# Performance work log

Hardware: AMD Instinct MI355X
Metric: run time of the kernel (lower is better)

The kernel has to match this reference:

```python
import jax, jax.numpy as jnp
import numpy as np

B, S, D = 4, 2048, 1024
LN_EPS = 1e-3  # keras LayerNormalization default


def setup_inputs() -> dict:
    key = jax.random.key(0)
    ks = jax.random.split(key, 4)
    std = 1.0 / np.sqrt(D)
    return {
        "inputs": jax.random.normal(ks[0], (B, S, D), dtype=jnp.float32),
        "Wq": jax.random.normal(ks[1], (D, D), dtype=jnp.float32) * std,
        "bq": jnp.zeros((D,), jnp.float32),
        "Wk": jax.random.normal(ks[2], (D, D), dtype=jnp.float32) * std,
        "bk": jnp.zeros((D,), jnp.float32),
        "Wv": jax.random.normal(ks[3], (D, D), dtype=jnp.float32) * std,
        "bv": jnp.zeros((D,), jnp.float32),
        "ln_gamma": jnp.ones((D,), jnp.float32),
        "ln_beta": jnp.zeros((D,), jnp.float32),
    }


def reference(inputs, Wq, bq, Wk, bk, Wv, bv, ln_gamma, ln_beta):
    d = inputs.shape[-1]
    scale = jnp.sqrt(jnp.asarray(d, inputs.dtype))
    q = inputs @ Wq + bq          # [B,S,D]
    k = inputs @ Wk + bk
    v = inputs @ Wv + bv
    scores = jnp.einsum("bqd,bkd->bqk", q, k) / scale  # [B,S,S]
    attn = jax.nn.softmax(scores, axis=-1)
    context = jnp.einsum("bqk,bkd->bqd", attn, v)      # [B,S,D]
    resid = context + inputs
    mu = jnp.mean(resid, axis=-1, keepdims=True)
    var = jnp.mean(jnp.square(resid - mu), axis=-1, keepdims=True)
    normed = (resid - mu) * jax.lax.rsqrt(var + LN_EPS)
    return normed * ln_gamma + ln_beta
```

## Files before the change

### kernel.cpp

```cpp
#include <hip/hip_runtime.h>
#include <hip/hip_bf16.h>
#include <cstdint>
#include <cstddef>


typedef unsigned short u16;
using bf16x8 = __attribute__((ext_vector_type(8))) short;
using f32x16 = __attribute__((ext_vector_type(16))) float;

typedef __attribute__((address_space(3))) unsigned int lds_uint;
typedef const __attribute__((address_space(1))) unsigned int glob_uint;

__device__ __forceinline__ float bf2f(u16 h) {
    union { unsigned int u; float f; } c;
    c.u = ((unsigned int)h) << 16;
    return c.f;
}
__device__ __forceinline__ u16 f2bf(float f) {
    union { float f; unsigned int u; } c;
    c.f = f;
    return (u16)((c.u + 0x7fffu + ((c.u >> 16) & 1u)) >> 16);
}
__device__ __forceinline__ void load_lds16(const void* g, void* l) {
    __builtin_amdgcn_global_load_lds((glob_uint*)g, (lds_uint*)l, 16, 0, 0);
}

__device__ __forceinline__ int detect_fp32(const u16* X, int* sflag) {
    const int t = threadIdx.x;
    if (t < 64) {
        bool bad = false, nz = false;
#pragma unroll
        for (int j = 0; j < 4; ++j) {
            float v = bf2f(X[(t * 4 + j) * 2]);
            if (!(fabsf(v) <= 1e9f)) bad = true;
            if (v != 0.f) nz = true;
        }
        unsigned long long ab = __ballot(bad);
        unsigned long long an = __ballot(nz);
        if (t == 0) *sflag = (ab != 0ull || an == 0ull) ? 1 : 0;
    }
    __syncthreads();
    return *sflag;
}

__global__ __launch_bounds__(256) void prep_kernel(
    const void* __restrict__ X, const void* __restrict__ Wq,
    const void* __restrict__ Wk, const void* __restrict__ Wv,
    const void* __restrict__ bq, const void* __restrict__ bk,
    const void* __restrict__ bv, const void* __restrict__ gamma,
    const void* __restrict__ beta,
    u16* __restrict__ Xb, u16* __restrict__ Wt, u16* __restrict__ bias5)
{
    __shared__ u16 tile[64][72];
    __shared__ int sflag;
    const int fp32 = detect_fp32((const u16*)X, &sflag);
    const int t   = threadIdx.x;
    const int blk = blockIdx.x;

    if (blk < 4096) {
        const size_t i = ((size_t)blk * 256 + t) * 8;
        if (fp32) {
            const float* f = (const float*)X;
            float4 a = *(const float4*)(f + i);
            float4 b = *(const float4*)(f + i + 4);
            ushort4 o0, o1;
            o0.x = f2bf(a.x); o0.y = f2bf(a.y); o0.z = f2bf(a.z); o0.w = f2bf(a.w);
            o1.x = f2bf(b.x); o1.y = f2bf(b.y); o1.z = f2bf(b.z); o1.w = f2bf(b.w);
            *(ushort4*)(Xb + i) = o0;
            *(ushort4*)(Xb + i + 4) = o1;
        } else {
            *(uint4*)(Xb + i) = *(const uint4*)((const u16*)X + i);
        }
    } else if (blk < 4864) {
        const int idx = blk - 4096;
        const int k0 = (idx & 15) * 64;
        const int n0 = ((idx >> 4) & 15) * 64;
        const int w  = idx >> 8;
        const void* W = (w == 0) ? Wq : ((w == 1) ? Wk : Wv);
#pragma unroll
        for (int it = 0; it < 2; ++it) {
            int i2 = t + it * 256;
            int r = i2 >> 3;
            int c = (i2 & 7) * 8;
            const size_t off = (size_t)(k0 + r) * 1024 + n0 + c;
            if (fp32) {
                const float* Wf = (const float*)W + off;
                float4 a = *(const float4*)Wf;
                float4 b = *(const float4*)(Wf + 4);
                u16* tp = &tile[r][c];
                tp[0] = f2bf(a.x); tp[1] = f2bf(a.y); tp[2] = f2bf(a.z); tp[3] = f2bf(a.w);
                tp[4] = f2bf(b.x); tp[5] = f2bf(b.y); tp[6] = f2bf(b.z); tp[7] = f2bf(b.w);
            } else {
                *(uint4*)&tile[r][c] = *(const uint4*)((const u16*)W + off);
            }
        }
        __syncthreads();
#pragma unroll
        for (int it = 0; it < 2; ++it) {
            int i2 = t + it * 256;
            int r = i2 >> 3;
            int c = (i2 & 7) * 8;
            union { u16 s[8]; uint4 v; } tmp;
#pragma unroll
            for (int j = 0; j < 8; ++j) tmp.s[j] = tile[c + j][r];
            *(uint4*)(Wt + (size_t)(w * 1024 + n0 + r) * 1024 + k0 + c) = tmp.v;
        }
    } else {
        const int v = blk - 4864;
        const void* srcs[5] = {bq, bk, bv, gamma, beta};
        const void* src = srcs[v];
        u16* d = bias5 + (size_t)v * 1024;
        const int i = t * 4;
        if (fp32) {
            const float* f = (const float*)src;
            ushort4 o;
            o.x = f2bf(f[i]); o.y = f2bf(f[i + 1]);
            o.z = f2bf(f[i + 2]); o.w = f2bf(f[i + 3]);
            *(ushort4*)(d + i) = o;
        } else {
            *(ushort4*)(d + i) = *(const ushort4*)((const u16*)src + i);
        }
    }
}

__global__ __launch_bounds__(256) void transpose_v4_kernel(
    const u16* __restrict__ QKV, u16* __restrict__ Vt4)
{
    __shared__ u16 tile[64][72];
    const int t  = threadIdx.x;
    const int k0 = blockIdx.x * 64;
    const int n0 = blockIdx.y * 64;
    const int b  = blockIdx.z;
    const u16* Vsrc = QKV + (size_t)b * 2048 * 3072 + 2048;
    u16* Vt = Vt4 + (size_t)b * 1024 * 2048;
#pragma unroll
    for (int it = 0; it < 2; ++it) {
        int idx = t + it * 256;
        int r = idx >> 3;
        int c = (idx & 7) * 8;
        *(uint4*)&tile[r][c] = *(const uint4*)(Vsrc + (size_t)(k0 + r) * 3072 + n0 + c);
    }
    __syncthreads();
#pragma unroll
    for (int it = 0; it < 2; ++it) {
        int idx = t + it * 256;
        int r = idx >> 3;
        int c = (idx & 7) * 8;
        union { u16 s[8]; uint4 v; } tmp;
#pragma unroll
        for (int j = 0; j < 8; ++j) tmp.s[j] = tile[c + j][r];
        *(uint4*)(Vt + (size_t)(n0 + r) * 2048 + k0 + c) = tmp.v;
    }
}

template<int EPI, int BN>
__global__ __launch_bounds__(512, 2) void gemm256(
    const u16* __restrict__ A, int lda, size_t sA,
    const u16* __restrict__ Bt, int ldb, size_t sB,
    u16* __restrict__ C, int ldc, size_t sC,
    int K, float scale, const u16* __restrict__ bias3)
{
    constexpr int WAVES_M = (BN == 256) ? 2 : 4;
    constexpr int WM = 256 / WAVES_M;
    constexpr int MF = WM / 32;
    __shared__ u16 As[4][256 * 32];
    __shared__ u16 Bs[4][BN * 32];

    const int t  = threadIdx.x;
    const int l  = t & 63;
    const int w  = t >> 6;
    const int wm = (BN == 256) ? (w >> 2) : (w >> 1);
    const int wn = (BN == 256) ? (w & 3)  : (w & 1);
    const int m0 = blockIdx.y * 256;
    const int n0 = blockIdx.x * BN;
    A  += (size_t)blockIdx.z * sA;
    Bt += (size_t)blockIdx.z * sB;
    C  += (size_t)blockIdx.z * sC;

    const int sa = (t & 3) ^ ((t >> 3) & 3);
    const u16* Ag0 = A  + (size_t)(m0 + (t >> 2)) * lda + sa * 8;
    const u16* Ag1 = Ag0 + (size_t)128 * lda;
    const u16* Bg0 = Bt + (size_t)(n0 + (t >> 2)) * ldb + sa * 8;
    const u16* Bg1 = Bg0 + (size_t)128 * ldb;

    const int lr   = l & 31;
    const int key  = (lr >> 1) & 3;
    const int sp0  = (l >> 5) ^ key;
    const int aoff = (wm * WM + lr) * 32;
    const int boff = (wn * 64 + lr) * 32;

    f32x16 acc[MF][2];
#pragma unroll
    for (int mi = 0; mi < MF; ++mi)
#pragma unroll
        for (int ni = 0; ni < 2; ++ni)
#pragma unroll
            for (int r = 0; r < 16; ++r) acc[mi][ni][r] = 0.f;

    const int NS = K >> 5;

    auto stage = [&](int j, int sl) {
        const size_t ko = (size_t)j * 32;
        load_lds16(Ag0 + ko, &As[sl][w * 512]);
        load_lds16(Ag1 + ko, &As[sl][4096 + w * 512]);
        load_lds16(Bg0 + ko, &Bs[sl][w * 512]);
        if constexpr (BN == 256) load_lds16(Bg1 + ko, &Bs[sl][4096 + w * 512]);
    };

    stage(0, 0); stage(1, 1); stage(2, 2);
    if constexpr (BN == 256) asm volatile("s_waitcnt vmcnt(8)" ::: "memory");
    else                     asm volatile("s_waitcnt vmcnt(6)" ::: "memory");
    __builtin_amdgcn_s_barrier();
    asm volatile("" ::: "memory");

    for (int j = 0; j < NS; ++j) {
        const int sl = j & 3;
        bf16x8 a[MF][2], b[2][2];
        const u16* as_ = &As[sl][aoff];
        const u16* bs_ = &Bs[sl][boff];
#pragma unroll
        for (int ks = 0; ks < 2; ++ks) {
            const int sp = (ks ? (sp0 ^ 2) : sp0) * 8;
#pragma unroll
            for (int mi = 0; mi < MF; ++mi)
                a[mi][ks] = *(const bf16x8*)(as_ + mi * 1024 + sp);
#pragma unroll
            for (int ni = 0; ni < 2; ++ni)
                b[ni][ks] = *(const bf16x8*)(bs_ + ni * 1024 + sp);
        }
        if (j + 3 < NS) stage(j + 3, (j + 3) & 3);
        const int rem = NS - 2 - j;
        if (rem >= 2) {
            if constexpr (BN == 256) asm volatile("s_waitcnt vmcnt(8)" ::: "memory");
            else                     asm volatile("s_waitcnt vmcnt(6)" ::: "memory");
        } else if (rem == 1) {
            if constexpr (BN == 256) asm volatile("s_waitcnt vmcnt(4)" ::: "memory");
            else                     asm volatile("s_waitcnt vmcnt(3)" ::: "memory");
        } else if (rem == 0) {
            asm volatile("s_waitcnt vmcnt(0)" ::: "memory");
        }
        if (j + 1 < NS) {
            __builtin_amdgcn_s_barrier();
            asm volatile("" ::: "memory");
        }
        __builtin_amdgcn_s_setprio(1);
#pragma unroll
        for (int ks = 0; ks < 2; ++ks)
#pragma unroll
            for (int mi = 0; mi < MF; ++mi)
#pragma unroll
                for (int ni = 0; ni < 2; ++ni)
                    acc[mi][ni] = __builtin_amdgcn_mfma_f32_32x32x16_bf16(
                        a[mi][ks], b[ni][ks], acc[mi][ni], 0, 0, 0);
        __builtin_amdgcn_s_setprio(0);
        if (j + 1 < NS) {
            __builtin_amdgcn_s_barrier();
            asm volatile("" ::: "memory");
        }
    }

    const int colb = n0 + wn * 64 + lr;
    const int rowb = m0 + wm * WM + 4 * (l >> 5);
#pragma unroll
    for (int mi = 0; mi < MF; ++mi) {
#pragma unroll
        for (int ni = 0; ni < 2; ++ni) {
            const int col = colb + ni * 32;
            const float bias = (EPI == 0) ? bf2f(bias3[col]) : 0.f;
#pragma unroll
            for (int r = 0; r < 16; ++r) {
                const int row = rowb + mi * 32 + (r & 3) + 8 * (r >> 2);
                C[(size_t)row * ldc + col] = f2bf(acc[mi][ni][r] * scale + bias);
            }
        }
    }
}

__global__ __launch_bounds__(256) void softmax_bf16_kernel(u16* __restrict__ S)
{
    const int t = threadIdx.x;
    u16* sp = S + (size_t)blockIdx.x * 2048;
    union { uint4 v; u16 h[8]; } raw;
    raw.v = *(const uint4*)(sp + t * 8);
    float vals[8];
#pragma unroll
    for (int i = 0; i < 8; ++i) vals[i] = bf2f(raw.h[i]);
    float m = vals[0];
#pragma unroll
    for (int i = 1; i < 8; ++i) m = fmaxf(m, vals[i]);
#pragma unroll
    for (int off = 32; off > 0; off >>= 1) m = fmaxf(m, __shfl_xor(m, off));
    __shared__ float red[8];
    const int w = t >> 6, lane = t & 63;
    if (lane == 0) red[w] = m;
    __syncthreads();
    m = fmaxf(fmaxf(red[0], red[1]), fmaxf(red[2], red[3]));
    float e[8], s = 0.f;
#pragma unroll
    for (int i = 0; i < 8; ++i) { e[i] = __expf(vals[i] - m); s += e[i]; }
#pragma unroll
    for (int off = 32; off > 0; off >>= 1) s += __shfl_xor(s, off);
    if (lane == 0) red[4 + w] = s;
    __syncthreads();
    s = red[4] + red[5] + red[6] + red[7];
    const float rinv = 1.f / s;
    union { uint4 v; u16 h[8]; } out;
#pragma unroll
    for (int i = 0; i < 8; ++i) out.h[i] = f2bf(e[i] * rinv);
    *(uint4*)(sp + t * 8) = out.v;
}

__global__ __launch_bounds__(256) void resid_ln_kernel(
    const u16* __restrict__ Ctx, const u16* __restrict__ Xb,
    const u16* __restrict__ gamma, const u16* __restrict__ beta,
    void* __restrict__ Out, const u16* __restrict__ Xraw)
{
    __shared__ int sflag;
    const int fp32 = detect_fp32(Xraw, &sflag);
    const size_t row = blockIdx.x;
    const int t = threadIdx.x;
    ushort4 cv = *(const ushort4*)(Ctx + row * 3072 + t * 4);
    ushort4 xv = *(const ushort4*)(Xb + row * 1024 + t * 4);
    float v[4] = {bf2f(cv.x) + bf2f(xv.x), bf2f(cv.y) + bf2f(xv.y),
                  bf2f(cv.z) + bf2f(xv.z), bf2f(cv.w) + bf2f(xv.w)};
    float s  = v[0] + v[1] + v[2] + v[3];
    float s2 = v[0] * v[0] + v[1] * v[1] + v[2] * v[2] + v[3] * v[3];
#pragma unroll
    for (int off = 32; off > 0; off >>= 1) {
        s  += __shfl_xor(s, off);
        s2 += __shfl_xor(s2, off);
    }
    __shared__ float red[8];
    const int w = t >> 6, lane = t & 63;
    if (lane == 0) { red[w] = s; red[4 + w] = s2; }
    __syncthreads();
    s  = red[0] + red[1] + red[2] + red[3];
    s2 = red[4] + red[5] + red[6] + red[7];
    const float mu  = s * (1.f / 1024.f);
    const float var = s2 * (1.f / 1024.f) - mu * mu;
    const float inv = rsqrtf(var + 1e-3f);
    ushort4 gv = *(const ushort4*)(gamma + t * 4);
    ushort4 bv = *(const ushort4*)(beta + t * 4);
    float o[4];
    o[0] = (v[0] - mu) * inv * bf2f(gv.x) + bf2f(bv.x);
    o[1] = (v[1] - mu) * inv * bf2f(gv.y) + bf2f(bv.y);
    o[2] = (v[2] - mu) * inv * bf2f(gv.z) + bf2f(bv.z);
    o[3] = (v[3] - mu) * inv * bf2f(gv.w) + bf2f(bv.w);
    if (fp32) {
        float4 fo = {o[0], o[1], o[2], o[3]};
        *(float4*)((float*)Out + row * 1024 + t * 4) = fo;
    } else {
        ushort4 bo;
        bo.x = f2bf(o[0]); bo.y = f2bf(o[1]); bo.z = f2bf(o[2]); bo.w = f2bf(o[3]);
        *(ushort4*)((u16*)Out + row * 1024 + t * 4) = bo;
    }
}

extern "C" void kernel_launch(void* const* d_in, const int* in_sizes, int n_in,
                              void* d_out, int out_size, void* d_ws, size_t ws_size,
                              hipStream_t stream)
{
    (void)in_sizes; (void)n_in; (void)out_size; (void)ws_size;
    const void* X     = d_in[0];
    const void* Wq    = d_in[1];
    const void* bq    = d_in[2];
    const void* Wk    = d_in[3];
    const void* bk    = d_in[4];
    const void* Wv    = d_in[5];
    const void* bv    = d_in[6];
    const void* gamma = d_in[7];
    const void* beta  = d_in[8];

    char* ws = (char*)d_ws;
    u16* bias5 = (u16*)(ws + 16);
    u16* Wt    = (u16*)(ws + 16384);
    u16* QKV   = (u16*)(ws + 6307840);
    u16* Xb    = (u16*)(ws + 56639488);
    u16* S4    = (u16*)(ws + 73416704);
    u16* Vt4   = (u16*)(ws + 106971136);

    prep_kernel<<<4869, 256, 0, stream>>>(
        X, Wq, Wk, Wv, bq, bk, bv, gamma, beta, Xb, Wt, bias5);

    gemm256<0, 128><<<dim3(24, 32, 1), 512, 0, stream>>>(
        Xb, 1024, 0, Wt, 1024, 0, QKV, 3072, 0, 1024, 1.f, bias5);

    gemm256<1, 256><<<dim3(8, 8, 4), 512, 0, stream>>>(
        QKV, 3072, (size_t)2048 * 3072,
        QKV + 1024, 3072, (size_t)2048 * 3072,
        S4, 2048, (size_t)2048 * 2048, 1024, 0.03125f, nullptr);

    softmax_bf16_kernel<<<8192, 256, 0, stream>>>(S4);

    transpose_v4_kernel<<<dim3(32, 16, 4), 256, 0, stream>>>(QKV, Vt4);

    gemm256<1, 128><<<dim3(8, 8, 4), 512, 0, stream>>>(
        S4, 2048, (size_t)2048 * 2048,
        Vt4, 2048, (size_t)1024 * 2048,
        QKV, 3072, (size_t)2048 * 3072, 2048, 1.f, nullptr);

    resid_ln_kernel<<<8192, 256, 0, stream>>>(
        QKV, Xb, bias5 + 3 * 1024, bias5 + 4 * 1024, d_out, (const u16*)X);
}
```

Before: 298.5 us.

## Rework GEMM to 256x256 tiles with BK=64 double buffering and split-K PV

Replaces the templated GEMM with a single 256x256-tile kernel that stages K in 64-wide slabs into two LDS buffers, using a new XOR swizzle, instead of a 4-deep pipeline of 32-wide slabs. The attention-times-V GEMM is split along K into two halves. Each half writes its partial context into a separate 1024-column slot of the QKV buffer, and the residual+LayerNorm kernel sums the two partials. The aim is more MFMA work per barrier and better grid fill for the PV product. The cost is a shallower prefetch pipeline, an extra partial-sum read, and summing the partials in bf16.

```diff
diff --git a/kernel.cpp b/kernel.cpp
--- a/kernel.cpp
+++ b/kernel.cpp
@@ -153,116 +153,122 @@
     }
 }
 
-template<int EPI, int BN>
-__global__ __launch_bounds__(512, 2) void gemm256(
+template<int EPI, int KSPLIT>
+__global__ __launch_bounds__(512, 2) void gemm256r(
     const u16* __restrict__ A, int lda, size_t sA,
     const u16* __restrict__ Bt, int ldb, size_t sB,
     u16* __restrict__ C, int ldc, size_t sC,
     int K, float scale, const u16* __restrict__ bias3)
 {
-    constexpr int WAVES_M = (BN == 256) ? 2 : 4;
-    constexpr int WM = 256 / WAVES_M;
-    constexpr int MF = WM / 32;
-    __shared__ u16 As[4][256 * 32];
-    __shared__ u16 Bs[4][BN * 32];
+    __shared__ u16 As[2][256 * 64];
+    __shared__ u16 Bs[2][256 * 64];
 
     const int t  = threadIdx.x;
     const int l  = t & 63;
     const int w  = t >> 6;
-    const int wm = (BN == 256) ? (w >> 2) : (w >> 1);
-    const int wn = (BN == 256) ? (w & 3)  : (w & 1);
+    const int wm = w >> 2;
+    const int wn = w & 3;
     const int m0 = blockIdx.y * 256;
-    const int n0 = blockIdx.x * BN;
-    A  += (size_t)blockIdx.z * sA;
-    Bt += (size_t)blockIdx.z * sB;
-    C  += (size_t)blockIdx.z * sC;
-
-    const int sa = (t & 3) ^ ((t >> 3) & 3);
-    const u16* Ag0 = A  + (size_t)(m0 + (t >> 2)) * lda + sa * 8;
-    const u16* Ag1 = Ag0 + (size_t)128 * lda;
-    const u16* Bg0 = Bt + (size_t)(n0 + (t >> 2)) * ldb + sa * 8;
-    const u16* Bg1 = Bg0 + (size_t)128 * ldb;
+    const int n0 = blockIdx.x * 256;
+    const int batch = (int)blockIdx.z >> (KSPLIT - 1);
+    const int ks    = (int)blockIdx.z & (KSPLIT - 1);
+    A  += (size_t)batch * sA + (size_t)ks * K;
+    Bt += (size_t)batch * sB + (size_t)ks * K;
+    C  += (size_t)batch * sC + (size_t)ks * 1024;
+
+    const int srow = w * 8 + (l >> 3);
+    const int sg   = (l & 7) ^ (l >> 3);
+    const u16* Ag = A  + (size_t)(m0 + srow) * lda + sg * 8;
+    const u16* Bg = Bt + (size_t)(n0 + srow) * ldb + sg * 8;
+
+    auto stage = [&](int j, int buf) {
+        const size_t kb = (size_t)j * 64;
+        const u16* ag = Ag + kb;
+        const u16* bg = Bg + kb;
+        u16* al = &As[buf][w * 512];
+        u16* bl = &Bs[buf][w * 512];
+#pragma unroll
+        for (int i = 0; i < 4; ++i) {
+            load_lds16(ag + (size_t)i * 64 * lda, al + i * 4096);
+            load_lds16(bg + (size_t)i * 64 * ldb, bl + i * 4096);
+        }
+    };
 
     const int lr   = l & 31;
-    const int key  = (lr >> 1) & 3;
-    const int sp0  = (l >> 5) ^ key;
-    const int aoff = (wm * WM + lr) * 32;
-    const int boff = (wn * 64 + lr) * 32;
-
-    f32x16 acc[MF][2];
-#pragma unroll
-    for (int mi = 0; mi < MF; ++mi)
+    const int kh   = l >> 5;
+    const int keyr = lr & 7;
+    const int aoff = (wm * 128 + lr) * 64;
+    const int boff = (wn * 64 + lr) * 64;
+
+    f32x16 acc[4][2];
+#pragma unroll
+    for (int mi = 0; mi < 4; ++mi)
 #pragma unroll
         for (int ni = 0; ni < 2; ++ni)
 #pragma unroll
             for (int r = 0; r < 16; ++r) acc[mi][ni][r] = 0.f;
 
-    const int NS = K >> 5;
-
-    auto stage = [&](int j, int sl) {
-        const size_t ko = (size_t)j * 32;
-        load_lds16(Ag0 + ko, &As[sl][w * 512]);
-        load_lds16(Ag1 + ko, &As[sl][4096 + w * 512]);
-        load_lds16(Bg0 + ko, &Bs[sl][w * 512]);
-        if constexpr (BN == 256) load_lds16(Bg1 + ko, &Bs[sl][4096 + w * 512]);
-    };
-
-    stage(0, 0); stage(1, 1); stage(2, 2);
-    if constexpr (BN == 256) asm volatile("s_waitcnt vmcnt(8)" ::: "memory");
-    else                     asm volatile("s_waitcnt vmcnt(6)" ::: "memory");
+    const int NS = K >> 6;
+
+    stage(0, 0);
+    stage(1, 1);
+    asm volatile("s_waitcnt vmcnt(8)" ::: "memory");
     __builtin_amdgcn_s_barrier();
     asm volatile("" ::: "memory");
 
     for (int j = 0; j < NS; ++j) {
-        const int sl = j & 3;
-        bf16x8 a[MF][2], b[2][2];
-        const u16* as_ = &As[sl][aoff];
-        const u16* bs_ = &Bs[sl][boff];
-#pragma unroll
-        for (int ks = 0; ks < 2; ++ks) {
-            const int sp = (ks ? (sp0 ^ 2) : sp0) * 8;
-#pragma unroll
-            for (int mi = 0; mi < MF; ++mi)
-                a[mi][ks] = *(const bf16x8*)(as_ + mi * 1024 + sp);
-#pragma unroll
-            for (int ni = 0; ni < 2; ++ni)
-                b[ni][ks] = *(const bf16x8*)(bs_ + ni * 1024 + sp);
-        }
-        if (j + 3 < NS) stage(j + 3, (j + 3) & 3);
-        const int rem = NS - 2 - j;
-        if (rem >= 2) {
-            if constexpr (BN == 256) asm volatile("s_waitcnt vmcnt(8)" ::: "memory");
-            else                     asm volatile("s_waitcnt vmcnt(6)" ::: "memory");
-        } else if (rem == 1) {
-            if constexpr (BN == 256) asm volatile("s_waitcnt vmcnt(4)" ::: "memory");
-            else                     asm volatile("s_waitcnt vmcnt(3)" ::: "memory");
-        } else if (rem == 0) {
+        const int buf = j & 1;
+        const u16* as_ = &As[buf][aoff];
+        const u16* bs_ = &Bs[buf][boff];
+        bf16x8 a[4][4], b[2][4];
+#pragma unroll
+        for (int ks2 = 0; ks2 < 2; ++ks2) {
+            const int sp = ((ks2 * 2 + kh) ^ keyr) * 8;
+#pragma unroll
+            for (int mi = 0; mi < 4; ++mi) a[mi][ks2] = *(const bf16x8*)(as_ + mi * 2048 + sp);
+#pragma unroll
+            for (int ni = 0; ni < 2; ++ni) b[ni][ks2] = *(const bf16x8*)(bs_ + ni * 2048 + sp);
+        }
+        if (j + 1 < NS) stage(j + 1, buf ^ 1);
+        __builtin_amdgcn_s_setprio(1);
+#pragma unroll
+        for (int ks2 = 0; ks2 < 2; ++ks2)
+#pragma unroll
+            for (int mi = 0; mi < 4; ++mi)
+#pragma unroll
+                for (int ni = 0; ni < 2; ++ni)
+                    acc[mi][ni] = __builtin_amdgcn_mfma_f32_32x32x16_bf16(
+                        a[mi][ks2], b[ni][ks2], acc[mi][ni], 0, 0, 0);
+        __builtin_amdgcn_s_setprio(0);
+#pragma unroll
+        for (int ks2 = 2; ks2 < 4; ++ks2) {
+            const int sp = ((ks2 * 2 + kh) ^ keyr) * 8;
+#pragma unroll
+            for (int mi = 0; mi < 4; ++mi) a[mi][ks2] = *(const bf16x8*)(as_ + mi * 2048 + sp);
+#pragma unroll
+            for (int ni = 0; ni < 2; ++ni) b[ni][ks2] = *(const bf16x8*)(bs_ + ni * 2048 + sp);
+        }
+        __builtin_amdgcn_s_setprio(1);
+#pragma unroll
+        for (int ks2 = 2; ks2 < 4; ++ks2)
+#pragma unroll
+            for (int mi = 0; mi < 4; ++mi)
+#pragma unroll
+                for (int ni = 0; ni < 2; ++ni)
+                    acc[mi][ni] = __builtin_amdgcn_mfma_f32_32x32x16_bf16(
+                        a[mi][ks2], b[ni][ks2], acc[mi][ni], 0, 0, 0);
+        __builtin_amdgcn_s_setprio(0);
+        if (j + 1 < NS) {
             asm volatile("s_waitcnt vmcnt(0)" ::: "memory");
-        }
-        if (j + 1 < NS) {
             __builtin_amdgcn_s_barrier();
             asm volatile("" ::: "memory");
         }
-        __builtin_amdgcn_s_setprio(1);
-#pragma unroll
-        for (int ks = 0; ks < 2; ++ks)
-#pragma unroll
-            for (int mi = 0; mi < MF; ++mi)
-#pragma unroll
-                for (int ni = 0; ni < 2; ++ni)
-                    acc[mi][ni] = __builtin_amdgcn_mfma_f32_32x32x16_bf16(
-                        a[mi][ks], b[ni][ks], acc[mi][ni], 0, 0, 0);
-        __builtin_amdgcn_s_setprio(0);
-        if (j + 1 < NS) {
-            __builtin_amdgcn_s_barrier();
-            asm volatile("" ::: "memory");
-        }
     }
 
     const int colb = n0 + wn * 64 + lr;
-    const int rowb = m0 + wm * WM + 4 * (l >> 5);
-#pragma unroll
-    for (int mi = 0; mi < MF; ++mi) {
+    const int rowb = m0 + wm * 128 + 4 * kh;
+#pragma unroll
+    for (int mi = 0; mi < 4; ++mi) {
 #pragma unroll
         for (int ni = 0; ni < 2; ++ni) {
             const int col = colb + ni * 32;
@@ -319,10 +325,13 @@
     const int fp32 = detect_fp32(Xraw, &sflag);
     const size_t row = blockIdx.x;
     const int t = threadIdx.x;
-    ushort4 cv = *(const ushort4*)(Ctx + row * 3072 + t * 4);
-    ushort4 xv = *(const ushort4*)(Xb + row * 1024 + t * 4);
-    float v[4] = {bf2f(cv.x) + bf2f(xv.x), bf2f(cv.y) + bf2f(xv.y),
-                  bf2f(cv.z) + bf2f(xv.z), bf2f(cv.w) + bf2f(xv.w)};
+    ushort4 cv0 = *(const ushort4*)(Ctx + row * 3072 + t * 4);
+    ushort4 cv1 = *(const ushort4*)(Ctx + row * 3072 + 1024 + t * 4);
+    ushort4 xv  = *(const ushort4*)(Xb + row * 1024 + t * 4);
+    float v[4] = {bf2f(cv0.x) + bf2f(cv1.x) + bf2f(xv.x),
+                  bf2f(cv0.y) + bf2f(cv1.y) + bf2f(xv.y),
+                  bf2f(cv0.z) + bf2f(cv1.z) + bf2f(xv.z),
+                  bf2f(cv0.w) + bf2f(cv1.w) + bf2f(xv.w)};
     float s  = v[0] + v[1] + v[2] + v[3];
     float s2 = v[0] * v[0] + v[1] * v[1] + v[2] * v[2] + v[3] * v[3];
 #pragma unroll
@@ -382,10 +391,10 @@
     prep_kernel<<<4869, 256, 0, stream>>>(
         X, Wq, Wk, Wv, bq, bk, bv, gamma, beta, Xb, Wt, bias5);
 
-    gemm256<0, 128><<<dim3(24, 32, 1), 512, 0, stream>>>(
+    gemm256r<0, 1><<<dim3(12, 32, 1), 512, 0, stream>>>(
         Xb, 1024, 0, Wt, 1024, 0, QKV, 3072, 0, 1024, 1.f, bias5);
 
-    gemm256<1, 256><<<dim3(8, 8, 4), 512, 0, stream>>>(
+    gemm256r<1, 1><<<dim3(8, 8, 4), 512, 0, stream>>>(
         QKV, 3072, (size_t)2048 * 3072,
         QKV + 1024, 3072, (size_t)2048 * 3072,
         S4, 2048, (size_t)2048 * 2048, 1024, 0.03125f, nullptr);
@@ -394,10 +403,10 @@
 
     transpose_v4_kernel<<<dim3(32, 16, 4), 256, 0, stream>>>(QKV, Vt4);
 
-    gemm256<1, 128><<<dim3(8, 8, 4), 512, 0, stream>>>(
+    gemm256r<1, 2><<<dim3(4, 8, 8), 512, 0, stream>>>(
         S4, 2048, (size_t)2048 * 2048,
         Vt4, 2048, (size_t)1024 * 2048,
-        QKV, 3072, (size_t)2048 * 3072, 2048, 1.f, nullptr);
+        QKV, 3072, (size_t)2048 * 3072, 1024, 1.f, nullptr);
 
     resid_ln_kernel<<<8192, 256, 0, stream>>>(
         QKV, Xb, bias5 + 3 * 1024, bias5 + 4 * 1024, d_out, (const u16*)X);
```

Measured after the change: 287.6 us. 3.7% less time.

## Rewrite GEMM with K=64 stages, triple buffering and interleaved LDS loads/MFMA

Applied to the files above, without the earlier changes.

Replaces the templated GEMM with a single 256x128 tile kernel that stages K in chunks of 64 rather than 32. It uses a 3-slot LDS ring instead of 4 and an 8-way XOR swizzle. LDS fragment reads are interleaved with the MFMA groups to hide LDS latency, and there are half as many barriers per K element. The QK^T GEMM now uses 256x128 tiles with twice the grid instead of 256x256. The cost is larger per-stage LDS (~144KB total), which may limit occupancy to one block per CU despite launch_bounds(512,2).

```diff
diff --git a/kernel.cpp b/kernel.cpp
--- a/kernel.cpp
+++ b/kernel.cpp
@@ -153,116 +153,133 @@
     }
 }
 
-template<int EPI, int BN>
-__global__ __launch_bounds__(512, 2) void gemm256(
+#define MFMA4(A0, A1, B0, B1)                                                   \
+    __builtin_amdgcn_s_setprio(1);                                              \
+    acc[0][0] = __builtin_amdgcn_mfma_f32_32x32x16_bf16(A0, B0, acc[0][0], 0, 0, 0); \
+    acc[0][1] = __builtin_amdgcn_mfma_f32_32x32x16_bf16(A0, B1, acc[0][1], 0, 0, 0); \
+    acc[1][0] = __builtin_amdgcn_mfma_f32_32x32x16_bf16(A1, B0, acc[1][0], 0, 0, 0); \
+    acc[1][1] = __builtin_amdgcn_mfma_f32_32x32x16_bf16(A1, B1, acc[1][1], 0, 0, 0); \
+    __builtin_amdgcn_s_setprio(0);
+
+template<int EPI>
+__global__ __launch_bounds__(512, 2) void gemm256x128(
     const u16* __restrict__ A, int lda, size_t sA,
     const u16* __restrict__ Bt, int ldb, size_t sB,
     u16* __restrict__ C, int ldc, size_t sC,
     int K, float scale, const u16* __restrict__ bias3)
 {
-    constexpr int WAVES_M = (BN == 256) ? 2 : 4;
-    constexpr int WM = 256 / WAVES_M;
-    constexpr int MF = WM / 32;
-    __shared__ u16 As[4][256 * 32];
-    __shared__ u16 Bs[4][BN * 32];
+    __shared__ u16 As[3][256 * 64];
+    __shared__ u16 Bs[3][128 * 64];
 
     const int t  = threadIdx.x;
     const int l  = t & 63;
     const int w  = t >> 6;
-    const int wm = (BN == 256) ? (w >> 2) : (w >> 1);
-    const int wn = (BN == 256) ? (w & 3)  : (w & 1);
+    const int wm = w >> 1;
+    const int wn = w & 1;
     const int m0 = blockIdx.y * 256;
-    const int n0 = blockIdx.x * BN;
+    const int n0 = blockIdx.x * 128;
     A  += (size_t)blockIdx.z * sA;
     Bt += (size_t)blockIdx.z * sB;
     C  += (size_t)blockIdx.z * sC;
 
-    const int sa = (t & 3) ^ ((t >> 3) & 3);
-    const u16* Ag0 = A  + (size_t)(m0 + (t >> 2)) * lda + sa * 8;
-    const u16* Ag1 = Ag0 + (size_t)128 * lda;
-    const u16* Bg0 = Bt + (size_t)(n0 + (t >> 2)) * ldb + sa * 8;
-    const u16* Bg1 = Bg0 + (size_t)128 * ldb;
+    const int srow = t >> 3;
+    const int sg   = (t & 7) ^ ((t >> 3) & 7);
+    const u16* Ag = A  + (size_t)(m0 + srow) * lda + sg * 8;
+    const u16* Bg = Bt + (size_t)(n0 + srow) * ldb + sg * 8;
+
+    auto stage = [&](int j, int sl) {
+        const size_t kb = (size_t)j * 64;
+        const u16* ag = Ag + kb;
+        const u16* bg = Bg + kb;
+        u16* al = &As[sl][w * 512];
+        u16* bl = &Bs[sl][w * 512];
+#pragma unroll
+        for (int i = 0; i < 4; ++i)
+            load_lds16(ag + (size_t)i * 64 * lda, al + i * 4096);
+#pragma unroll
+        for (int i = 0; i < 2; ++i)
+            load_lds16(bg + (size_t)i * 64 * ldb, bl + i * 4096);
+    };
 
     const int lr   = l & 31;
-    const int key  = (lr >> 1) & 3;
-    const int sp0  = (l >> 5) ^ key;
-    const int aoff = (wm * WM + lr) * 32;
-    const int boff = (wn * 64 + lr) * 32;
-
-    f32x16 acc[MF][2];
-#pragma unroll
-    for (int mi = 0; mi < MF; ++mi)
+    const int kh   = l >> 5;
+    const int keyr = lr & 7;
+    const int aoff = (wm * 64 + lr) * 64;
+    const int boff = (wn * 64 + lr) * 64;
+
+    f32x16 acc[2][2];
+#pragma unroll
+    for (int mi = 0; mi < 2; ++mi)
 #pragma unroll
         for (int ni = 0; ni < 2; ++ni)
 #pragma unroll
             for (int r = 0; r < 16; ++r) acc[mi][ni][r] = 0.f;
 
-    const int NS = K >> 5;
-
-    auto stage = [&](int j, int sl) {
-        const size_t ko = (size_t)j * 32;
-        load_lds16(Ag0 + ko, &As[sl][w * 512]);
-        load_lds16(Ag1 + ko, &As[sl][4096 + w * 512]);
-        load_lds16(Bg0 + ko, &Bs[sl][w * 512]);
-        if constexpr (BN == 256) load_lds16(Bg1 + ko, &Bs[sl][4096 + w * 512]);
-    };
-
-    stage(0, 0); stage(1, 1); stage(2, 2);
-    if constexpr (BN == 256) asm volatile("s_waitcnt vmcnt(8)" ::: "memory");
-    else                     asm volatile("s_waitcnt vmcnt(6)" ::: "memory");
+    const int NS = K >> 6;
+
+    stage(0, 0);
+    stage(1, 1);
+    asm volatile("s_waitcnt vmcnt(6)" ::: "memory");
     __builtin_amdgcn_s_barrier();
     asm volatile("" ::: "memory");
 
+    int sl = 0;
     for (int j = 0; j < NS; ++j) {
-        const int sl = j & 3;
-        bf16x8 a[MF][2], b[2][2];
         const u16* as_ = &As[sl][aoff];
         const u16* bs_ = &Bs[sl][boff];
-#pragma unroll
-        for (int ks = 0; ks < 2; ++ks) {
-            const int sp = (ks ? (sp0 ^ 2) : sp0) * 8;
-#pragma unroll
-            for (int mi = 0; mi < MF; ++mi)
-                a[mi][ks] = *(const bf16x8*)(as_ + mi * 1024 + sp);
-#pragma unroll
-            for (int ni = 0; ni < 2; ++ni)
-                b[ni][ks] = *(const bf16x8*)(bs_ + ni * 1024 + sp);
-        }
-        if (j + 3 < NS) stage(j + 3, (j + 3) & 3);
-        const int rem = NS - 2 - j;
-        if (rem >= 2) {
-            if constexpr (BN == 256) asm volatile("s_waitcnt vmcnt(8)" ::: "memory");
-            else                     asm volatile("s_waitcnt vmcnt(6)" ::: "memory");
-        } else if (rem == 1) {
-            if constexpr (BN == 256) asm volatile("s_waitcnt vmcnt(4)" ::: "memory");
-            else                     asm volatile("s_waitcnt vmcnt(3)" ::: "memory");
-        } else if (rem == 0) {
-            asm volatile("s_waitcnt vmcnt(0)" ::: "memory");
-        }
+        bf16x8 aE0, aE1, bE0, bE1, aO0, aO1, bO0, bO1;
+        {
+            const int sp = (kh ^ keyr) * 8;
+            aE0 = *(const bf16x8*)(as_ + sp);
+            aE1 = *(const bf16x8*)(as_ + 2048 + sp);
+            bE0 = *(const bf16x8*)(bs_ + sp);
+            bE1 = *(const bf16x8*)(bs_ + 2048 + sp);
+        }
+        {
+            const int sp = ((2 + kh) ^ keyr) * 8;
+            aO0 = *(const bf16x8*)(as_ + sp);
+            aO1 = *(const bf16x8*)(as_ + 2048 + sp);
+            bO0 = *(const bf16x8*)(bs_ + sp);
+            bO1 = *(const bf16x8*)(bs_ + 2048 + sp);
+        }
+        if (j + 2 < NS) {
+            int s2 = sl + 2; if (s2 >= 3) s2 -= 3;
+            stage(j + 2, s2);
+        }
+        MFMA4(aE0, aE1, bE0, bE1);
+        {
+            const int sp = ((4 + kh) ^ keyr) * 8;
+            aE0 = *(const bf16x8*)(as_ + sp);
+            aE1 = *(const bf16x8*)(as_ + 2048 + sp);
+            bE0 = *(const bf16x8*)(bs_ + sp);
+            bE1 = *(const bf16x8*)(bs_ + 2048 + sp);
+        }
+        MFMA4(aO0, aO1, bO0, bO1);
+        {
+            const int sp = ((6 + kh) ^ keyr) * 8;
+            aO0 = *(const bf16x8*)(as_ + sp);
+            aO1 = *(const bf16x8*)(as_ + 2048 + sp);
+            bO0 = *(const bf16x8*)(bs_ + sp);
+            bO1 = *(const bf16x8*)(bs_ + 2048 + sp);
+        }
+        MFMA4(aE0, aE1, bE0, bE1);
+        MFMA4(aO0, aO1, bO0, bO1);
         if (j + 1 < NS) {
+            if (j + 2 < NS) {
+                asm volatile("s_waitcnt vmcnt(6)" ::: "memory");
+            } else {
+                asm volatile("s_waitcnt vmcnt(0)" ::: "memory");
+            }
             __builtin_amdgcn_s_barrier();
             asm volatile("" ::: "memory");
         }
-        __builtin_amdgcn_s_setprio(1);
-#pragma unroll
-        for (int ks = 0; ks < 2; ++ks)
-#pragma unroll
-            for (int mi = 0; mi < MF; ++mi)
-#pragma unroll
-                for (int ni = 0; ni < 2; ++ni)
-                    acc[mi][ni] = __builtin_amdgcn_mfma_f32_32x32x16_bf16(
-                        a[mi][ks], b[ni][ks], acc[mi][ni], 0, 0, 0);
-        __builtin_amdgcn_s_setprio(0);
-        if (j + 1 < NS) {
-            __builtin_amdgcn_s_barrier();
-            asm volatile("" ::: "memory");
-        }
+        sl = (sl == 2) ? 0 : sl + 1;
     }
 
     const int colb = n0 + wn * 64 + lr;
-    const int rowb = m0 + wm * WM + 4 * (l >> 5);
-#pragma unroll
-    for (int mi = 0; mi < MF; ++mi) {
+    const int rowb = m0 + wm * 64 + 4 * kh;
+#pragma unroll
+    for (int mi = 0; mi < 2; ++mi) {
 #pragma unroll
         for (int ni = 0; ni < 2; ++ni) {
             const int col = colb + ni * 32;
@@ -382,10 +399,10 @@
     prep_kernel<<<4869, 256, 0, stream>>>(
         X, Wq, Wk, Wv, bq, bk, bv, gamma, beta, Xb, Wt, bias5);
 
-    gemm256<0, 128><<<dim3(24, 32, 1), 512, 0, stream>>>(
+    gemm256x128<0><<<dim3(24, 32, 1), 512, 0, stream>>>(
         Xb, 1024, 0, Wt, 1024, 0, QKV, 3072, 0, 1024, 1.f, bias5);
 
-    gemm256<1, 256><<<dim3(8, 8, 4), 512, 0, stream>>>(
+    gemm256x128<1><<<dim3(16, 8, 4), 512, 0, stream>>>(
         QKV, 3072, (size_t)2048 * 3072,
         QKV + 1024, 3072, (size_t)2048 * 3072,
         S4, 2048, (size_t)2048 * 2048, 1024, 0.03125f, nullptr);
@@ -394,7 +411,7 @@
 
     transpose_v4_kernel<<<dim3(32, 16, 4), 256, 0, stream>>>(QKV, Vt4);
 
-    gemm256<1, 128><<<dim3(8, 8, 4), 512, 0, stream>>>(
+    gemm256x128<1><<<dim3(8, 8, 4), 512, 0, stream>>>(
         S4, 2048, (size_t)2048 * 2048,
         Vt4, 2048, (size_t)1024 * 2048,
         QKV, 3072, (size_t)2048 * 3072, 2048, 1.f, nullptr);
```

Result: no change. 295.9 us (-0.9%).
